# Kernel tuning notes

Hardware: AMD Instinct MI355X
Metric: run time of the kernel (lower is better)

Reference implementation:

```python
import jax, jax.numpy as jnp
import numpy as np

B, T, DM, DFE, DH, DRH = 32, 2048, 128, 64, 64, 64
E, NF, NSF, TOPK = 8, 16, 64, 2
LN_EPS = 1e-5


def setup_inputs() -> dict:
    key = jax.random.key(0)
    ks = jax.random.split(key, 18)
    s = 0.05
    # base expert i owns columns [16*i, 16*i+16); scale=2 -> expert e uses base e//2
    expert_idx = jnp.asarray(np.stack([np.arange(NF) + NF * (e // 2) for e in range(E)]), dtype=jnp.int32)  # [E,NF]
    stage_idx = jnp.arange(NSF, dtype=jnp.int32)  # stage uses all 64 columns
    return {
        'hidden': jax.random.normal(ks[0], (B, T, DM), jnp.float32),
        'feat': jax.random.normal(ks[1], (B, T, NSF), jnp.float32),
        'ln_g': jnp.ones((DM,), jnp.float32),
        'ln_b': jnp.zeros((DM,), jnp.float32),
        'Wp': jax.random.normal(ks[2], (NSF, DFE), jnp.float32) * s,
        'bp': jnp.zeros((DFE,), jnp.float32),
        'Wr1': jax.random.normal(ks[3], (DM + DFE, DRH), jnp.float32) * s,
        'br1': jnp.zeros((DRH,), jnp.float32),
        'Wr2': jax.random.normal(ks[4], (DRH, E), jnp.float32) * s,
        'br2': jnp.zeros((E,), jnp.float32),
        'Wf': jax.random.normal(ks[5], (E, NF, DFE), jnp.float32) * s,
        'bf': jnp.zeros((E, DFE), jnp.float32),
        'We1h': jax.random.normal(ks[6], (E, DM, DH), jnp.float32) * s,
        'We1f': jax.random.normal(ks[7], (E, DFE, DH), jnp.float32) * s,
        'be1': jnp.zeros((E, DH), jnp.float32),
        'We2': jax.random.normal(ks[8], (E, DH, DM), jnp.float32) * s,
        'be2': jnp.zeros((E, DM), jnp.float32),
        'alpha': jnp.asarray(1.0, jnp.float32),
        'item_seq_len': jax.random.randint(ks[9], (B,), 1, T + 1),
        'expert_idx': expert_idx,
        'stage_idx': stage_idx,
    }


def _layernorm(x, g, b):
    mu = jnp.mean(x, -1, keepdims=True)
    v = jnp.mean(jnp.square(x - mu), -1, keepdims=True)
    return (x - mu) * jax.lax.rsqrt(v + LN_EPS) * g + b


def reference(hidden, feat, ln_g, ln_b, Wp, bp, Wr1, br1, Wr2, br2,
              Wf, bf, We1h, We1f, be1, We2, be2, alpha,
              item_seq_len, expert_idx, stage_idx):
    h = _layernorm(hidden, ln_g, ln_b)                         # [B,T,DM]  pre_ln
    femb = feat[..., stage_idx] @ Wp + bp                      # [B,T,DFE] stage feature projection
    # --- token router: MLP -> softmax(temp=1) -> top-k renormalized gates ---
    rin = jnp.concatenate([h, femb], -1)                       # [B,T,DM+DFE]
    logits = jax.nn.relu(rin @ Wr1 + br1) @ Wr2 + br2          # [B,T,E]
    probs = jax.nn.softmax(logits, axis=-1)
    topv, topi = jax.lax.top_k(probs, TOPK)                    # [B,T,K]
    topv = topv / jnp.sum(topv, -1, keepdims=True)
    gates = jnp.sum(jax.nn.one_hot(topi, E, dtype=probs.dtype) * topv[..., None], axis=-2)  # [B,T,E]
    valid = jnp.arange(T)[None, :] < item_seq_len[:, None]     # [B,T]
    gates = gates * valid[..., None].astype(gates.dtype)
    # --- experts: per-expert feature gather + 2-layer GELU MLP (hidden + feat inputs) ---
    ef = feat[:, :, expert_idx]                                # [B,T,E,NF] gather
    x = jnp.einsum('btef,efd->bted', ef, Wf) + bf              # [B,T,E,DFE]
    h1 = jax.nn.gelu(jnp.einsum('btd,edo->bteo', h, We1h)
                     + jnp.einsum('bted,edo->bteo', x, We1f) + be1, approximate=False)
    eo = jnp.einsum('bteo,eod->bted', h1, We2) + be2           # [B,T,E,DM]
    moe = jnp.einsum('bte,bted->btd', gates, eo)               # weighted combine
    next_hidden = hidden + alpha * moe                         # residual, alpha_scale=1, dropout=0
    return next_hidden, gates, probs
```

## Files before the change

kernel.cpp:

```cpp
#include <hip/hip_runtime.h>
#include <hip/hip_bf16.h>


typedef unsigned short u16;
typedef __attribute__((ext_vector_type(8))) short bfrag;
typedef __attribute__((ext_vector_type(8))) u16 u16x8;
typedef __attribute__((ext_vector_type(4))) float facc;
typedef __attribute__((ext_vector_type(4))) float f32x4;

#define NTOK 65536
#define CAP 65536

#define OFF_CNT   ((size_t)0)
#define OFF_LTOK  ((size_t)256)
#define OFF_LGATE (OFF_LTOK + 2097152)
#define OFF_HWS   (OFF_LGATE + 2097152)
#define OFF_W1T   (OFF_HWS + 16777216)
#define OFF_W2T   (OFF_W1T + 196608)
#define OFF_B1P   (OFF_W2T + 131072)
#define OFF_WPR   (OFF_B1P + 2048)
#define OFF_BR1P  (OFF_WPR + 16384)

__device__ __forceinline__ u16 f2bf(float f) {
  union { __hip_bfloat16 h; u16 u; } cv;
  cv.h = __float2bfloat16(f);
  return cv.u;
}

__global__ __launch_bounds__(256)
void k0_pre(const float* __restrict__ Wp, const float* __restrict__ bp,
            const float* __restrict__ Wr1, const float* __restrict__ br1,
            const float* __restrict__ Wf, const float* __restrict__ bfv,
            const float* __restrict__ We1h, const float* __restrict__ We1f,
            const float* __restrict__ be1, const float* __restrict__ We2,
            float* __restrict__ Wpr, float* __restrict__ br1p,
            u16* __restrict__ w1t, u16* __restrict__ w2t, float* __restrict__ b1p)
{
  int j = blockIdx.x * 256 + threadIdx.x;
  if (j < 4096) {
    int i = j >> 6, o = j & 63;
    float s = 0.f;
    for (int k = 0; k < 64; ++k) s += Wp[i*64+k] * Wr1[(128+k)*64 + o];
    Wpr[i*64+o] = s;
  } else if (j < 4160) {
    int o = j - 4096;
    float s = br1[o];
    for (int k = 0; k < 64; ++k) s += bp[k] * Wr1[(128+k)*64 + o];
    br1p[o] = s;
  } else if (j < 4160 + 98304) {
    int idx = j - 4160;
    int e = idx / 12288; int rem = idx % 12288;
    int jj = rem / 192; int k = rem % 192;
    float v = 0.f;
    if (k < 128) v = We1h[(e*128 + k)*64 + jj];
    else if (k < 144) {
      int i = k - 128; float s = 0.f;
      for (int d = 0; d < 64; ++d) s += Wf[(e*16+i)*64 + d] * We1f[(e*64+d)*64 + jj];
      v = s;
    }
    size_t byte = (size_t)(e*64 + jj)*384 + ((2*k) ^ ((jj & 7) << 4));
    *(u16*)((char*)w1t + byte) = f2bf(v);
  } else if (j < 4160 + 98304 + 65536) {
    int idx = j - 4160 - 98304;
    int e = idx / 8192; int rem = idx % 8192;
    int d = rem / 64; int k = rem & 63;
    float v = We2[(e*64 + k)*128 + d];
    size_t byte = (size_t)(e*128 + d)*128 + ((2*k) ^ ((d & 7) << 4));
    *(u16*)((char*)w2t + byte) = f2bf(v);
  } else if (j < 4160 + 98304 + 65536 + 512) {
    int idx = j - 4160 - 98304 - 65536;
    int e = idx >> 6, o = idx & 63;
    float s = be1[e*64 + o];
    for (int d = 0; d < 64; ++d) s += bfv[e*64 + d] * We1f[(e*64+d)*64 + o];
    b1p[e*64 + o] = s;
  }
}

__global__ __launch_bounds__(512)
void k1_router(const float* __restrict__ hidden, const float* __restrict__ feat,
               const float* __restrict__ ln_g, const float* __restrict__ ln_b,
               const float* __restrict__ Wr1, const float* __restrict__ Wr2,
               const float* __restrict__ br2, const int* __restrict__ seqlen,
               const int* __restrict__ sidx_g,
               const float* __restrict__ Wpr, const float* __restrict__ br1p,
               float* __restrict__ outN, float* __restrict__ outG, float* __restrict__ outP,
               u16* __restrict__ hws, int* __restrict__ cnt,
               int* __restrict__ listTok, float* __restrict__ listGate)
{
  __shared__ float At[64*128];
  __shared__ float Wc[64*64];
  __shared__ float sW2[64*8];
  __shared__ float sb1[64], sg[128], sb[128], sbr2[8];
  __shared__ int ssidx[64];
  __shared__ int lcnt[8], lbase[8];
  __shared__ int ltok[8][128];
  __shared__ float lgate[8][128];

  int tid = threadIdx.x;
  int w = tid >> 6, lane = tid & 63;

  if (tid < 512) sW2[tid] = Wr2[tid];
  if (tid < 64) { sb1[tid] = br1p[tid]; ssidx[tid] = sidx_g[tid]; }
  if (tid >= 64 && tid < 192) { int i = tid - 64; sg[i] = ln_g[i]; }
  if (tid >= 192 && tid < 320) { int i = tid - 192; sb[i] = ln_b[i]; }
  if (tid >= 320 && tid < 328) { sbr2[tid-320] = br2[tid-320]; }
  if (tid >= 328 && tid < 336) { lcnt[tid-328] = 0; }
  __syncthreads();

  int tbase = blockIdx.x * 128 + w * 16;

  float h0v[16], h1v[16], fv[16];
  #pragma unroll
  for (int p = 0; p < 8; ++p) {
    int tA = tbase + 2*p, tB = tA + 1;
    float xA0 = hidden[tA*128 + lane],      xA1 = hidden[tA*128 + 64 + lane];
    float xB0 = hidden[tB*128 + lane],      xB1 = hidden[tB*128 + 64 + lane];
    fv[2*p]   = feat[tA*64 + ssidx[lane]];
    fv[2*p+1] = feat[tB*64 + ssidx[lane]];
    outN[tA*128 + lane] = xA0; outN[tA*128 + 64 + lane] = xA1;
    outN[tB*128 + lane] = xB0; outN[tB*128 + 64 + lane] = xB1;
    float sA = xA0 + xA1, sB = xB0 + xB1;
    #pragma unroll
    for (int m = 1; m < 64; m <<= 1) { sA += __shfl_xor(sA, m, 64); sB += __shfl_xor(sB, m, 64); }
    float muA = sA * (1.f/128.f), muB = sB * (1.f/128.f);
    float dA0 = xA0-muA, dA1 = xA1-muA, dB0 = xB0-muB, dB1 = xB1-muB;
    float qA = dA0*dA0 + dA1*dA1, qB = dB0*dB0 + dB1*dB1;
    #pragma unroll
    for (int m = 1; m < 64; m <<= 1) { qA += __shfl_xor(qA, m, 64); qB += __shfl_xor(qB, m, 64); }
    float rsA = rsqrtf(qA*(1.f/128.f) + 1e-5f), rsB = rsqrtf(qB*(1.f/128.f) + 1e-5f);
    float hA0 = dA0*rsA*sg[lane]    + sb[lane],    hA1 = dA1*rsA*sg[64+lane] + sb[64+lane];
    float hB0 = dB0*rsB*sg[lane]    + sb[lane],    hB1 = dB1*rsB*sg[64+lane] + sb[64+lane];
    hws[tA*128 + lane] = f2bf(hA0); hws[tA*128 + 64 + lane] = f2bf(hA1);
    hws[tB*128 + lane] = f2bf(hB0); hws[tB*128 + 64 + lane] = f2bf(hB1);
    h0v[2*p] = hA0; h1v[2*p] = hA1; h0v[2*p+1] = hB0; h1v[2*p+1] = hB1;
  }

  float acc[4][4];
  #pragma unroll
  for (int i = 0; i < 4; ++i)
    #pragma unroll
    for (int q = 0; q < 4; ++q) acc[i][q] = 0.f;

  int tb = w*4 + (lane >> 4);
  int ob = (lane & 15) * 4;

  #pragma unroll 1
  for (int c = 0; c < 3; ++c) {
    __syncthreads();
    const float* wsrc = (c == 0) ? Wr1 : (c == 1) ? (Wr1 + 64*64) : Wpr;
    for (int i = tid; i < 1024; i += 512) ((f32x4*)Wc)[i] = ((const f32x4*)wsrc)[i];
    #pragma unroll
    for (int tk = 0; tk < 16; ++tk) {
      int tl = w*16 + tk;
      float v = (c == 0) ? h0v[tk] : (c == 1) ? h1v[tk] : fv[tk];
      int byte = (lane << 9) + (((((tl >> 2) ^ (lane & 15))) << 4) | ((tl & 3) << 2));
      *(float*)((char*)At + byte) = v;
    }
    __syncthreads();
    #pragma unroll 4
    for (int k = 0; k < 64; ++k) {
      f32x4 a4 = *(const f32x4*)((const char*)At + (k << 9) + ((tb ^ (k & 15)) << 4));
      f32x4 b4 = *(const f32x4*)(Wc + k*64 + ob);
      #pragma unroll
      for (int i = 0; i < 4; ++i)
        #pragma unroll
        for (int q = 0; q < 4; ++q)
          acc[i][q] = fmaf(a4[i], b4[q], acc[i][q]);
    }
  }

  float w2r[4][8];
  #pragma unroll
  for (int q = 0; q < 4; ++q)
    #pragma unroll
    for (int e = 0; e < 8; ++e) w2r[q][e] = sW2[(ob + q)*8 + e];
  float b1r[4];
  #pragma unroll
  for (int q = 0; q < 4; ++q) b1r[q] = sb1[ob + q];

  int j = lane & 15;
  #pragma unroll 1
  for (int ti = 0; ti < 4; ++ti) {
    float lo[8];
    #pragma unroll
    for (int e = 0; e < 8; ++e) lo[e] = 0.f;
    #pragma unroll
    for (int q = 0; q < 4; ++q) {
      float z = fmaxf(acc[ti][q] + b1r[q], 0.f);
      #pragma unroll
      for (int e = 0; e < 8; ++e) lo[e] = fmaf(z, w2r[q][e], lo[e]);
    }
    #pragma unroll
    for (int m = 1; m < 16; m <<= 1) {
      #pragma unroll
      for (int e = 0; e < 8; ++e) lo[e] += __shfl_xor(lo[e], m, 64);
    }
    #pragma unroll
    for (int e = 0; e < 8; ++e) lo[e] += sbr2[e];

    int t = tbase + (lane >> 4)*4 + ti;
    float mx = lo[0];
    #pragma unroll
    for (int e = 1; e < 8; ++e) mx = fmaxf(mx, lo[e]);
    float ex[8]; float s = 0.f;
    #pragma unroll
    for (int e = 0; e < 8; ++e) { ex[e] = __expf(lo[e] - mx); s += ex[e]; }
    float inv = 1.f / s;
    float p[8];
    #pragma unroll
    for (int e = 0; e < 8; ++e) p[e] = ex[e] * inv;
    float p1 = p[0]; int i1 = 0;
    #pragma unroll
    for (int e = 1; e < 8; ++e) { bool tk2 = p[e] > p1; p1 = tk2 ? p[e] : p1; i1 = tk2 ? e : i1; }
    float p2 = -1.f; int i2 = 0;
    #pragma unroll
    for (int e = 0; e < 8; ++e) { bool tk2 = (e != i1) && (p[e] > p2); p2 = tk2 ? p[e] : p2; i2 = tk2 ? e : i2; }
    int bb = t >> 11, tt = t & 2047;
    bool valid = tt < seqlen[bb];
    float gden = 1.f / (p1 + p2);
    float g1 = p1 * gden, g2 = p2 * gden;
    float pv = p[0];
    #pragma unroll
    for (int e = 1; e < 8; ++e) pv = (j == e) ? p[e] : pv;
    if (j < 8) outP[t*8 + j] = pv;
    float gv = (j == i1) ? g1 : ((j == i2) ? g2 : 0.f);
    if (!valid) gv = 0.f;
    if (j < 8) outG[t*8 + j] = gv;
    if (valid && j == 0) {
      int lp = atomicAdd(&lcnt[i1], 1); ltok[i1][lp] = t; lgate[i1][lp] = g1;
      lp = atomicAdd(&lcnt[i2], 1); ltok[i2][lp] = t; lgate[i2][lp] = g2;
    }
  }

  __syncthreads();
  if (tid < 8) lbase[tid] = atomicAdd(&cnt[tid], lcnt[tid]);
  __syncthreads();
  #pragma unroll 1
  for (int e = 0; e < 8; ++e) {
    int ncnt = lcnt[e];
    if (tid < ncnt) {
      listTok[e*CAP + lbase[e] + tid] = ltok[e][tid];
      listGate[e*CAP + lbase[e] + tid] = lgate[e][tid];
    }
  }
}

__global__ __launch_bounds__(256)
void k2_experts(const float* __restrict__ feat, const u16* __restrict__ hws,
                const u16* __restrict__ w1t, const u16* __restrict__ w2t,
                const float* __restrict__ b1p, const float* __restrict__ be2,
                const float* __restrict__ alphap, const int* __restrict__ eidx_g,
                const int* __restrict__ cnt, const int* __restrict__ listTok,
                const float* __restrict__ listGate, float* __restrict__ outN)
{
  __shared__ u16 Xs[64*192];
  __shared__ u16 W1s[64*192];
  __shared__ u16 W2s[128*64];
  __shared__ u16 H1s[64*64];
  __shared__ float b1s[64], be2s[128], gts[64];
  __shared__ int toks[64];
  __shared__ int seidx[16];

  int e = blockIdx.x >> 10;
  int seg = blockIdx.x & 1023;
  int n = cnt[e];
  int row0 = seg << 6;
  if (row0 >= n) return;
  int nr = n - row0; if (nr > 64) nr = 64;
  int tid = threadIdx.x;

  if (tid < 64) {
    int tok = 0; float gt = 0.f;
    if (tid < nr) { tok = listTok[e*CAP + row0 + tid]; gt = listGate[e*CAP + row0 + tid]; }
    toks[tid] = tok; gts[tid] = gt;
    b1s[tid] = b1p[e*64 + tid];
  }
  if (tid >= 64 && tid < 192) be2s[tid - 64] = be2[e*128 + tid - 64];
  if (tid < 16) seidx[tid] = eidx_g[e*16 + tid];
  {
    const u16x8* s1 = (const u16x8*)(w1t + e*64*192);
    u16x8* d1 = (u16x8*)W1s;
    for (int i = tid; i < 1536; i += 256) d1[i] = s1[i];
    const u16x8* s2 = (const u16x8*)(w2t + e*128*64);
    u16x8* d2 = (u16x8*)W2s;
    for (int i = tid; i < 1024; i += 256) d2[i] = s2[i];
  }
  __syncthreads();
  for (int c = tid; c < 1024; c += 256) {
    int r = c >> 4, p = c & 15;
    u16x8 v = *(const u16x8*)(hws + toks[r]*128 + p*8);
    *(u16x8*)((char*)Xs + r*384 + ((p*16) ^ ((r & 7) << 4))) = v;
  }
  if (tid < 128) {
    int r = tid >> 1, hf = tid & 1;
    int tok = toks[r];
    u16x8 ov;
    #pragma unroll
    for (int q = 0; q < 8; ++q) ov[q] = f2bf(feat[tok*64 + seidx[hf*8 + q]]);
    *(u16x8*)((char*)Xs + r*384 + ((256 + hf*16) ^ ((r & 7) << 4))) = ov;
    u16x8 zv = {0,0,0,0,0,0,0,0};
    *(u16x8*)((char*)Xs + r*384 + ((288 + hf*16) ^ ((r & 7) << 4))) = zv;
  }
  __syncthreads();

  int w = tid >> 6, lane = tid & 63;
  int la = lane & 15, lg = lane >> 4;
  int wm = (w >> 1) * 32, wn = (w & 1) * 32;

  facc acc[2][2];
  #pragma unroll
  for (int a = 0; a < 2; ++a)
    #pragma unroll
    for (int b2 = 0; b2 < 2; ++b2) { facc z = {0.f,0.f,0.f,0.f}; acc[a][b2] = z; }
  #pragma unroll
  for (int kc = 0; kc < 5; ++kc) {
    int kb = kc*64 + lg*16;
    bfrag af[2], bf2[2];
    #pragma unroll
    for (int mi = 0; mi < 2; ++mi) {
      int r = wm + mi*16 + la;
      af[mi] = *(const bfrag*)((const char*)Xs + r*384 + (kb ^ ((r & 7) << 4)));
    }
    #pragma unroll
    for (int ni = 0; ni < 2; ++ni) {
      int r = wn + ni*16 + la;
      bf2[ni] = *(const bfrag*)((const char*)W1s + r*384 + (kb ^ ((r & 7) << 4)));
    }
    #pragma unroll
    for (int mi = 0; mi < 2; ++mi)
      #pragma unroll
      for (int ni = 0; ni < 2; ++ni)
        acc[mi][ni] = __builtin_amdgcn_mfma_f32_16x16x32_bf16(af[mi], bf2[ni], acc[mi][ni], 0, 0, 0);
  }
  #pragma unroll
  for (int mi = 0; mi < 2; ++mi)
    #pragma unroll
    for (int ni = 0; ni < 2; ++ni)
      #pragma unroll
      for (int rg = 0; rg < 4; ++rg) {
        int r = wm + mi*16 + lg*4 + rg;
        int c = wn + ni*16 + la;
        float z = acc[mi][ni][rg] + b1s[c];
        float gl = 0.5f * z * (1.f + erff(z * 0.70710678118f));
        *(u16*)((char*)H1s + r*128 + ((2*c) ^ ((r & 7) << 4))) = f2bf(gl);
      }
  __syncthreads();

  facc acc2[2][4];
  #pragma unroll
  for (int a = 0; a < 2; ++a)
    #pragma unroll
    for (int b2 = 0; b2 < 4; ++b2) { facc z = {0.f,0.f,0.f,0.f}; acc2[a][b2] = z; }
  int wn2 = (w & 1) * 64;
  #pragma unroll
  for (int kc = 0; kc < 2; ++kc) {
    int kb = kc*64 + lg*16;
    bfrag af[2], bf2[4];
    #pragma unroll
    for (int mi = 0; mi < 2; ++mi) {
      int r = wm + mi*16 + la;
      af[mi] = *(const bfrag*)((const char*)H1s + r*128 + (kb ^ ((r & 7) << 4)));
    }
    #pragma unroll
    for (int ni = 0; ni < 4; ++ni) {
      int r = wn2 + ni*16 + la;
      bf2[ni] = *(const bfrag*)((const char*)W2s + r*128 + (kb ^ ((r & 7) << 4)));
    }
    #pragma unroll
    for (int mi = 0; mi < 2; ++mi)
      #pragma unroll
      for (int ni = 0; ni < 4; ++ni)
        acc2[mi][ni] = __builtin_amdgcn_mfma_f32_16x16x32_bf16(af[mi], bf2[ni], acc2[mi][ni], 0, 0, 0);
  }
  float alpha = alphap[0];
  #pragma unroll
  for (int mi = 0; mi < 2; ++mi)
    #pragma unroll
    for (int ni = 0; ni < 4; ++ni)
      #pragma unroll
      for (int rg = 0; rg < 4; ++rg) {
        int r = wm + mi*16 + lg*4 + rg;
        int c = wn2 + ni*16 + la;
        float gt = gts[r];
        if (gt != 0.f) {
          float v = acc2[mi][ni][rg] + be2s[c];
          atomicAdd(outN + toks[r]*128 + c, alpha * gt * v);
        }
      }
}

extern "C" void kernel_launch(void* const* d_in, const int* in_sizes, int n_in,
                              void* d_out, int out_size, void* d_ws, size_t ws_size,
                              hipStream_t stream) {
  const float* hidden = (const float*)d_in[0];
  const float* feat   = (const float*)d_in[1];
  const float* ln_g   = (const float*)d_in[2];
  const float* ln_b   = (const float*)d_in[3];
  const float* Wp     = (const float*)d_in[4];
  const float* bp     = (const float*)d_in[5];
  const float* Wr1    = (const float*)d_in[6];
  const float* br1    = (const float*)d_in[7];
  const float* Wr2    = (const float*)d_in[8];
  const float* br2    = (const float*)d_in[9];
  const float* Wf     = (const float*)d_in[10];
  const float* bfv    = (const float*)d_in[11];
  const float* We1h   = (const float*)d_in[12];
  const float* We1f   = (const float*)d_in[13];
  const float* be1    = (const float*)d_in[14];
  const float* We2    = (const float*)d_in[15];
  const float* be2    = (const float*)d_in[16];
  const float* alpha  = (const float*)d_in[17];
  const int* seqlen   = (const int*)d_in[18];
  const int* eidx     = (const int*)d_in[19];
  const int* sidx     = (const int*)d_in[20];

  char* ws = (char*)d_ws;
  int*   cnt      = (int*)(ws + OFF_CNT);
  int*   listTok  = (int*)(ws + OFF_LTOK);
  float* listGate = (float*)(ws + OFF_LGATE);
  u16*   hws      = (u16*)(ws + OFF_HWS);
  u16*   w1t      = (u16*)(ws + OFF_W1T);
  u16*   w2t      = (u16*)(ws + OFF_W2T);
  float* b1p      = (float*)(ws + OFF_B1P);
  float* Wpr      = (float*)(ws + OFF_WPR);
  float* br1p     = (float*)(ws + OFF_BR1P);

  float* outN = (float*)d_out;
  float* outG = outN + (size_t)NTOK * 128;
  float* outP = outG + (size_t)NTOK * 8;

  hipMemsetAsync(ws + OFF_CNT, 0, 256, stream);
  k0_pre<<<659, 256, 0, stream>>>(Wp, bp, Wr1, br1, Wf, bfv, We1h, We1f, be1, We2,
                                  Wpr, br1p, w1t, w2t, b1p);
  k1_router<<<512, 512, 0, stream>>>(hidden, feat, ln_g, ln_b, Wr1, Wr2, br2, seqlen,
                                     sidx, Wpr, br1p, outN, outG, outP, hws, cnt,
                                     listTok, listGate);
  k2_experts<<<8192, 256, 0, stream>>>(feat, hws, w1t, w2t, b1p, be2, alpha, eidx,
                                       cnt, listTok, listGate, outN);
}
```

Measured before the change: 111.2 us.

## Replace atomic MoE scatter with per-slot expert outputs and separate combine kernel

```diff
diff --git a/kernel.cpp b/kernel.cpp
--- a/kernel.cpp
+++ b/kernel.cpp
@@ -12,10 +12,12 @@
 #define CAP 65536
 
 #define OFF_CNT   ((size_t)0)
-#define OFF_LTOK  ((size_t)256)
-#define OFF_LGATE (OFF_LTOK + 2097152)
-#define OFF_HWS   (OFF_LGATE + 2097152)
-#define OFF_W1T   (OFF_HWS + 16777216)
+#define OFF_SEGM  ((size_t)256)
+#define OFF_LTOK  ((size_t)512)
+#define OFF_SMAPG (OFF_LTOK + (size_t)8*CAP*4)
+#define OFF_HWS   (OFF_SMAPG + (size_t)NTOK*8)
+#define OFF_EOTOK (OFF_HWS + (size_t)NTOK*128*2)
+#define OFF_W1T   (OFF_EOTOK + (size_t)NTOK*2*128*2)
 #define OFF_W2T   (OFF_W1T + 196608)
 #define OFF_B1P   (OFF_W2T + 131072)
 #define OFF_WPR   (OFF_B1P + 2048)
@@ -25,6 +27,9 @@
   union { __hip_bfloat16 h; u16 u; } cv;
   cv.h = __float2bfloat16(f);
   return cv.u;
+}
+__device__ __forceinline__ float bf2f(u16 u) {
+  return __uint_as_float(((unsigned)u) << 16);
 }
 
 __global__ __launch_bounds__(256)
@@ -76,119 +81,139 @@
   }
 }
 
-__global__ __launch_bounds__(512)
+__global__ __launch_bounds__(256, 4)
 void k1_router(const float* __restrict__ hidden, const float* __restrict__ feat,
                const float* __restrict__ ln_g, const float* __restrict__ ln_b,
                const float* __restrict__ Wr1, const float* __restrict__ Wr2,
                const float* __restrict__ br2, const int* __restrict__ seqlen,
                const int* __restrict__ sidx_g,
                const float* __restrict__ Wpr, const float* __restrict__ br1p,
-               float* __restrict__ outN, float* __restrict__ outG, float* __restrict__ outP,
+               float* __restrict__ outG, float* __restrict__ outP,
                u16* __restrict__ hws, int* __restrict__ cnt,
-               int* __restrict__ listTok, float* __restrict__ listGate)
+               int* __restrict__ listTok, float* __restrict__ smapG)
 {
-  __shared__ float At[64*128];
+  __shared__ float At[64*64];
   __shared__ float Wc[64*64];
-  __shared__ float sW2[64*8];
+  __shared__ float sW2[512];
   __shared__ float sb1[64], sg[128], sb[128], sbr2[8];
   __shared__ int ssidx[64];
   __shared__ int lcnt[8], lbase[8];
-  __shared__ int ltok[8][128];
-  __shared__ float lgate[8][128];
+  __shared__ int ltok[8][64];
+  __shared__ float tg[64][2];
 
   int tid = threadIdx.x;
-  int w = tid >> 6, lane = tid & 63;
-
-  if (tid < 512) sW2[tid] = Wr2[tid];
+  for (int i = tid; i < 512; i += 256) sW2[i] = Wr2[i];
+  if (tid < 128) sg[tid] = ln_g[tid]; else sb[tid-128] = ln_b[tid-128];
   if (tid < 64) { sb1[tid] = br1p[tid]; ssidx[tid] = sidx_g[tid]; }
-  if (tid >= 64 && tid < 192) { int i = tid - 64; sg[i] = ln_g[i]; }
-  if (tid >= 192 && tid < 320) { int i = tid - 192; sb[i] = ln_b[i]; }
-  if (tid >= 320 && tid < 328) { sbr2[tid-320] = br2[tid-320]; }
-  if (tid >= 328 && tid < 336) { lcnt[tid-328] = 0; }
+  if (tid >= 64 && tid < 72) sbr2[tid-64] = br2[tid-64];
+  if (tid >= 72 && tid < 80) lcnt[tid-72] = 0;
   __syncthreads();
 
-  int tbase = blockIdx.x * 128 + w * 16;
-
-  float h0v[16], h1v[16], fv[16];
-  #pragma unroll
-  for (int p = 0; p < 8; ++p) {
-    int tA = tbase + 2*p, tB = tA + 1;
-    float xA0 = hidden[tA*128 + lane],      xA1 = hidden[tA*128 + 64 + lane];
-    float xB0 = hidden[tB*128 + lane],      xB1 = hidden[tB*128 + 64 + lane];
-    fv[2*p]   = feat[tA*64 + ssidx[lane]];
-    fv[2*p+1] = feat[tB*64 + ssidx[lane]];
-    outN[tA*128 + lane] = xA0; outN[tA*128 + 64 + lane] = xA1;
-    outN[tB*128 + lane] = xB0; outN[tB*128 + 64 + lane] = xB1;
-    float sA = xA0 + xA1, sB = xB0 + xB1;
-    #pragma unroll
-    for (int m = 1; m < 64; m <<= 1) { sA += __shfl_xor(sA, m, 64); sB += __shfl_xor(sB, m, 64); }
-    float muA = sA * (1.f/128.f), muB = sB * (1.f/128.f);
-    float dA0 = xA0-muA, dA1 = xA1-muA, dB0 = xB0-muB, dB1 = xB1-muB;
-    float qA = dA0*dA0 + dA1*dA1, qB = dB0*dB0 + dB1*dB1;
-    #pragma unroll
-    for (int m = 1; m < 64; m <<= 1) { qA += __shfl_xor(qA, m, 64); qB += __shfl_xor(qB, m, 64); }
-    float rsA = rsqrtf(qA*(1.f/128.f) + 1e-5f), rsB = rsqrtf(qB*(1.f/128.f) + 1e-5f);
-    float hA0 = dA0*rsA*sg[lane]    + sb[lane],    hA1 = dA1*rsA*sg[64+lane] + sb[64+lane];
-    float hB0 = dB0*rsB*sg[lane]    + sb[lane],    hB1 = dB1*rsB*sg[64+lane] + sb[64+lane];
-    hws[tA*128 + lane] = f2bf(hA0); hws[tA*128 + 64 + lane] = f2bf(hA1);
-    hws[tB*128 + lane] = f2bf(hB0); hws[tB*128 + 64 + lane] = f2bf(hB1);
-    h0v[2*p] = hA0; h1v[2*p] = hA1; h0v[2*p+1] = hB0; h1v[2*p+1] = hB1;
-  }
+  int tok = tid >> 2, q = tid & 3;
+  int t = blockIdx.x * 64 + tok;
+
+  f32x4 x[8];
+  #pragma unroll
+  for (int i = 0; i < 8; ++i) x[i] = *(const f32x4*)(hidden + (size_t)t*128 + q*32 + i*4);
+  float s = 0.f;
+  #pragma unroll
+  for (int i = 0; i < 8; ++i) { s += x[i][0] + x[i][1]; s += x[i][2] + x[i][3]; }
+  s += __shfl_xor(s, 1, 64); s += __shfl_xor(s, 2, 64);
+  float mu = s * (1.f/128.f);
+  float v = 0.f;
+  #pragma unroll
+  for (int i = 0; i < 8; ++i) {
+    #pragma unroll
+    for (int j = 0; j < 4; ++j) { float d = x[i][j] - mu; v = fmaf(d, d, v); }
+  }
+  v += __shfl_xor(v, 1, 64); v += __shfl_xor(v, 2, 64);
+  float rs = rsqrtf(v * (1.f/128.f) + 1e-5f);
+  #pragma unroll
+  for (int i = 0; i < 8; ++i) {
+    #pragma unroll
+    for (int j = 0; j < 4; ++j) {
+      int c = q*32 + i*4 + j;
+      x[i][j] = (x[i][j] - mu) * rs * sg[c] + sb[c];
+    }
+  }
+  #pragma unroll
+  for (int m = 0; m < 4; ++m) {
+    u16x8 o;
+    #pragma unroll
+    for (int j = 0; j < 4; ++j) { o[j] = f2bf(x[2*m][j]); o[4+j] = f2bf(x[2*m+1][j]); }
+    *(u16x8*)(hws + (size_t)t*128 + q*32 + m*8) = o;
+  }
+  float fv[16];
+  #pragma unroll
+  for (int i = 0; i < 16; ++i) fv[i] = feat[(size_t)t*64 + ssidx[q*16 + i]];
 
   float acc[4][4];
   #pragma unroll
   for (int i = 0; i < 4; ++i)
     #pragma unroll
-    for (int q = 0; q < 4; ++q) acc[i][q] = 0.f;
-
-  int tb = w*4 + (lane >> 4);
-  int ob = (lane & 15) * 4;
+    for (int p = 0; p < 4; ++p) acc[i][p] = 0.f;
+
+  int tb = tid >> 4;
+  int ob = (tid & 15) * 4;
 
   #pragma unroll 1
   for (int c = 0; c < 3; ++c) {
     __syncthreads();
-    const float* wsrc = (c == 0) ? Wr1 : (c == 1) ? (Wr1 + 64*64) : Wpr;
-    for (int i = tid; i < 1024; i += 512) ((f32x4*)Wc)[i] = ((const f32x4*)wsrc)[i];
-    #pragma unroll
-    for (int tk = 0; tk < 16; ++tk) {
-      int tl = w*16 + tk;
-      float v = (c == 0) ? h0v[tk] : (c == 1) ? h1v[tk] : fv[tk];
-      int byte = (lane << 9) + (((((tl >> 2) ^ (lane & 15))) << 4) | ((tl & 3) << 2));
-      *(float*)((char*)At + byte) = v;
-    }
+    if (c < 2) {
+      if ((c == 0) ? (q < 2) : (q >= 2)) {
+        int kbase = (c == 0) ? q*32 : (q-2)*32;
+        #pragma unroll
+        for (int i = 0; i < 8; ++i)
+          #pragma unroll
+          for (int j = 0; j < 4; ++j) {
+            int kr = kbase + i*4 + j;
+            int byte = (kr << 8) + ((((tok >> 2) ^ ((kr >> 2) & 15)) << 4) | ((tok & 3) << 2));
+            *(float*)((char*)At + byte) = x[i][j];
+          }
+      }
+    } else {
+      #pragma unroll
+      for (int i = 0; i < 16; ++i) {
+        int kr = q*16 + i;
+        int byte = (kr << 8) + ((((tok >> 2) ^ ((kr >> 2) & 15)) << 4) | ((tok & 3) << 2));
+        *(float*)((char*)At + byte) = fv[i];
+      }
+    }
+    const float* wsrc = (c == 0) ? Wr1 : (c == 1) ? (Wr1 + 4096) : Wpr;
+    for (int i = tid; i < 1024; i += 256) ((f32x4*)Wc)[i] = ((const f32x4*)wsrc)[i];
     __syncthreads();
     #pragma unroll 4
     for (int k = 0; k < 64; ++k) {
-      f32x4 a4 = *(const f32x4*)((const char*)At + (k << 9) + ((tb ^ (k & 15)) << 4));
+      f32x4 a4 = *(const f32x4*)((const char*)At + (k << 8) + ((tb ^ ((k >> 2) & 15)) << 4));
       f32x4 b4 = *(const f32x4*)(Wc + k*64 + ob);
       #pragma unroll
       for (int i = 0; i < 4; ++i)
         #pragma unroll
-        for (int q = 0; q < 4; ++q)
-          acc[i][q] = fmaf(a4[i], b4[q], acc[i][q]);
+        for (int p = 0; p < 4; ++p)
+          acc[i][p] = fmaf(a4[i], b4[p], acc[i][p]);
     }
   }
 
   float w2r[4][8];
   #pragma unroll
-  for (int q = 0; q < 4; ++q)
-    #pragma unroll
-    for (int e = 0; e < 8; ++e) w2r[q][e] = sW2[(ob + q)*8 + e];
+  for (int p = 0; p < 4; ++p)
+    #pragma unroll
+    for (int e = 0; e < 8; ++e) w2r[p][e] = sW2[(ob + p)*8 + e];
   float b1r[4];
   #pragma unroll
-  for (int q = 0; q < 4; ++q) b1r[q] = sb1[ob + q];
-
-  int j = lane & 15;
+  for (int p = 0; p < 4; ++p) b1r[p] = sb1[ob + p];
+
+  int j16 = tid & 15;
   #pragma unroll 1
   for (int ti = 0; ti < 4; ++ti) {
     float lo[8];
     #pragma unroll
     for (int e = 0; e < 8; ++e) lo[e] = 0.f;
     #pragma unroll
-    for (int q = 0; q < 4; ++q) {
-      float z = fmaxf(acc[ti][q] + b1r[q], 0.f);
-      #pragma unroll
-      for (int e = 0; e < 8; ++e) lo[e] = fmaf(z, w2r[q][e], lo[e]);
+    for (int p = 0; p < 4; ++p) {
+      float z = fmaxf(acc[ti][p] + b1r[p], 0.f);
+      #pragma unroll
+      for (int e = 0; e < 8; ++e) lo[e] = fmaf(z, w2r[p][e], lo[e]);
     }
     #pragma unroll
     for (int m = 1; m < 16; m <<= 1) {
@@ -198,14 +223,15 @@
     #pragma unroll
     for (int e = 0; e < 8; ++e) lo[e] += sbr2[e];
 
-    int t = tbase + (lane >> 4)*4 + ti;
+    int tloc = tb*4 + ti;
+    int tt = blockIdx.x*64 + tloc;
     float mx = lo[0];
     #pragma unroll
     for (int e = 1; e < 8; ++e) mx = fmaxf(mx, lo[e]);
-    float ex[8]; float s = 0.f;
-    #pragma unroll
-    for (int e = 0; e < 8; ++e) { ex[e] = __expf(lo[e] - mx); s += ex[e]; }
-    float inv = 1.f / s;
+    float ex[8]; float ss = 0.f;
+    #pragma unroll
+    for (int e = 0; e < 8; ++e) { ex[e] = __expf(lo[e] - mx); ss += ex[e]; }
+    float inv = 1.f / ss;
     float p[8];
     #pragma unroll
     for (int e = 0; e < 8; ++e) p[e] = ex[e] * inv;
@@ -215,20 +241,24 @@
     float p2 = -1.f; int i2 = 0;
     #pragma unroll
     for (int e = 0; e < 8; ++e) { bool tk2 = (e != i1) && (p[e] > p2); p2 = tk2 ? p[e] : p2; i2 = tk2 ? e : i2; }
-    int bb = t >> 11, tt = t & 2047;
-    bool valid = tt < seqlen[bb];
+    bool valid = (tt & 2047) < seqlen[tt >> 11];
     float gden = 1.f / (p1 + p2);
     float g1 = p1 * gden, g2 = p2 * gden;
     float pv = p[0];
     #pragma unroll
-    for (int e = 1; e < 8; ++e) pv = (j == e) ? p[e] : pv;
-    if (j < 8) outP[t*8 + j] = pv;
-    float gv = (j == i1) ? g1 : ((j == i2) ? g2 : 0.f);
+    for (int e = 1; e < 8; ++e) pv = (j16 == e) ? p[e] : pv;
+    if (j16 < 8) outP[(size_t)tt*8 + j16] = pv;
+    float gv = (j16 == i1) ? g1 : ((j16 == i2) ? g2 : 0.f);
     if (!valid) gv = 0.f;
-    if (j < 8) outG[t*8 + j] = gv;
-    if (valid && j == 0) {
-      int lp = atomicAdd(&lcnt[i1], 1); ltok[i1][lp] = t; lgate[i1][lp] = g1;
-      lp = atomicAdd(&lcnt[i2], 1); ltok[i2][lp] = t; lgate[i2][lp] = g2;
+    if (j16 < 8) outG[(size_t)tt*8 + j16] = gv;
+    if (j16 == 0) {
+      if (valid) {
+        int lp = atomicAdd(&lcnt[i1], 1); ltok[i1][lp] = (tt << 1);
+        lp = atomicAdd(&lcnt[i2], 1);     ltok[i2][lp] = (tt << 1) | 1;
+        tg[tloc][0] = g1; tg[tloc][1] = g2;
+      } else {
+        tg[tloc][0] = 0.f; tg[tloc][1] = 0.f;
+      }
     }
   }
 
@@ -238,10 +268,21 @@
   #pragma unroll 1
   for (int e = 0; e < 8; ++e) {
     int ncnt = lcnt[e];
-    if (tid < ncnt) {
-      listTok[e*CAP + lbase[e] + tid] = ltok[e][tid];
-      listGate[e*CAP + lbase[e] + tid] = lgate[e][tid];
-    }
+    if (tid < ncnt) listTok[(size_t)e*CAP + lbase[e] + tid] = ltok[e][tid];
+  }
+  if (tid < 64) {
+    float2 g; g.x = tg[tid][0]; g.y = tg[tid][1];
+    ((float2*)smapG)[blockIdx.x*64 + tid] = g;
+  }
+}
+
+__global__ void k1b_prefix(const int* __restrict__ cnt, int* __restrict__ segm)
+{
+  if (threadIdx.x == 0 && blockIdx.x == 0) {
+    int s = 0;
+    #pragma unroll
+    for (int e = 0; e < 8; ++e) { segm[e] = s; s += (cnt[e] + 63) >> 6; }
+    segm[8] = s;
   }
 }
 
@@ -249,34 +290,38 @@
 void k2_experts(const float* __restrict__ feat, const u16* __restrict__ hws,
                 const u16* __restrict__ w1t, const u16* __restrict__ w2t,
                 const float* __restrict__ b1p, const float* __restrict__ be2,
-                const float* __restrict__ alphap, const int* __restrict__ eidx_g,
-                const int* __restrict__ cnt, const int* __restrict__ listTok,
-                const float* __restrict__ listGate, float* __restrict__ outN)
+                const int* __restrict__ eidx_g, const int* __restrict__ cnt,
+                const int* __restrict__ segm, const int* __restrict__ listTok,
+                u16* __restrict__ eoTok)
 {
   __shared__ u16 Xs[64*192];
   __shared__ u16 W1s[64*192];
   __shared__ u16 W2s[128*64];
   __shared__ u16 H1s[64*64];
-  __shared__ float b1s[64], be2s[128], gts[64];
-  __shared__ int toks[64];
+  __shared__ float b1s[64], be2s[128];
+  __shared__ int sent[64];
   __shared__ int seidx[16];
-
-  int e = blockIdx.x >> 10;
-  int seg = blockIdx.x & 1023;
+  __shared__ int snr;
+
+  int b = blockIdx.x;
+  if (b >= segm[8]) return;
+  int e = 0;
+  #pragma unroll
+  for (int i = 1; i < 8; ++i) if (b >= segm[i]) e = i;
+  int row0 = (b - segm[e]) << 6;
   int n = cnt[e];
-  int row0 = seg << 6;
-  if (row0 >= n) return;
   int nr = n - row0; if (nr > 64) nr = 64;
   int tid = threadIdx.x;
+  if (tid == 0) snr = nr;
 
   if (tid < 64) {
-    int tok = 0; float gt = 0.f;
-    if (tid < nr) { tok = listTok[e*CAP + row0 + tid]; gt = listGate[e*CAP + row0 + tid]; }
-    toks[tid] = tok; gts[tid] = gt;
+    int ent = 0;
+    if (tid < nr) ent = listTok[(size_t)e*CAP + row0 + tid];
+    sent[tid] = ent;
     b1s[tid] = b1p[e*64 + tid];
   }
   if (tid >= 64 && tid < 192) be2s[tid - 64] = be2[e*128 + tid - 64];
-  if (tid < 16) seidx[tid] = eidx_g[e*16 + tid];
+  if (tid >= 192 && tid < 208) seidx[tid-192] = eidx_g[e*16 + tid - 192];
   {
     const u16x8* s1 = (const u16x8*)(w1t + e*64*192);
     u16x8* d1 = (u16x8*)W1s;
@@ -288,15 +333,15 @@
   __syncthreads();
   for (int c = tid; c < 1024; c += 256) {
     int r = c >> 4, p = c & 15;
-    u16x8 v = *(const u16x8*)(hws + toks[r]*128 + p*8);
+    u16x8 v = *(const u16x8*)(hws + (size_t)(sent[r] >> 1)*128 + p*8);
     *(u16x8*)((char*)Xs + r*384 + ((p*16) ^ ((r & 7) << 4))) = v;
   }
   if (tid < 128) {
     int r = tid >> 1, hf = tid & 1;
-    int tok = toks[r];
+    int tk = sent[r] >> 1;
     u16x8 ov;
     #pragma unroll
-    for (int q = 0; q < 8; ++q) ov[q] = f2bf(feat[tok*64 + seidx[hf*8 + q]]);
+    for (int p = 0; p < 8; ++p) ov[p] = f2bf(feat[(size_t)tk*64 + seidx[hf*8 + p]]);
     *(u16x8*)((char*)Xs + r*384 + ((256 + hf*16) ^ ((r & 7) << 4))) = ov;
     u16x8 zv = {0,0,0,0,0,0,0,0};
     *(u16x8*)((char*)Xs + r*384 + ((288 + hf*16) ^ ((r & 7) << 4))) = zv;
@@ -372,7 +417,6 @@
       for (int ni = 0; ni < 4; ++ni)
         acc2[mi][ni] = __builtin_amdgcn_mfma_f32_16x16x32_bf16(af[mi], bf2[ni], acc2[mi][ni], 0, 0, 0);
   }
-  float alpha = alphap[0];
   #pragma unroll
   for (int mi = 0; mi < 2; ++mi)
     #pragma unroll
@@ -381,12 +425,43 @@
       for (int rg = 0; rg < 4; ++rg) {
         int r = wm + mi*16 + lg*4 + rg;
         int c = wn2 + ni*16 + la;
-        float gt = gts[r];
-        if (gt != 0.f) {
+        if (r < snr) {
           float v = acc2[mi][ni][rg] + be2s[c];
-          atomicAdd(outN + toks[r]*128 + c, alpha * gt * v);
+          eoTok[(size_t)sent[r]*128 + c] = f2bf(v);
         }
       }
+}
+
+__global__ __launch_bounds__(256)
+void k3_combine(const float* __restrict__ hidden, const float* __restrict__ smapG,
+                const u16* __restrict__ eoTok, const float* __restrict__ alphap,
+                float* __restrict__ outN)
+{
+  int tid = threadIdx.x;
+  int tok = tid >> 2, q = tid & 3;
+  int t = blockIdx.x*64 + tok;
+  float2 g = ((const float2*)smapG)[t];
+  float a = alphap[0];
+  float ag0 = a * g.x, ag1 = a * g.y;
+  const f32x4* hp = (const f32x4*)(hidden + (size_t)t*128 + q*32);
+  f32x4* op = (f32x4*)(outN + (size_t)t*128 + q*32);
+  const u16x8* e0 = (const u16x8*)(eoTok + ((size_t)t*2)*128 + q*32);
+  const u16x8* e1 = (const u16x8*)(eoTok + ((size_t)t*2 + 1)*128 + q*32);
+  #pragma unroll
+  for (int i = 0; i < 4; ++i) {
+    f32x4 r0 = hp[2*i], r1 = hp[2*i+1];
+    if (g.x != 0.f) {
+      u16x8 x0 = e0[i];
+      #pragma unroll
+      for (int j = 0; j < 4; ++j) { r0[j] = fmaf(ag0, bf2f(x0[j]), r0[j]); r1[j] = fmaf(ag0, bf2f(x0[4+j]), r1[j]); }
+    }
+    if (g.y != 0.f) {
+      u16x8 x1 = e1[i];
+      #pragma unroll
+      for (int j = 0; j < 4; ++j) { r0[j] = fmaf(ag1, bf2f(x1[j]), r0[j]); r1[j] = fmaf(ag1, bf2f(x1[4+j]), r1[j]); }
+    }
+    op[2*i] = r0; op[2*i+1] = r1;
+  }
 }
 
 extern "C" void kernel_launch(void* const* d_in, const int* in_sizes, int n_in,
@@ -416,9 +491,11 @@
 
   char* ws = (char*)d_ws;
   int*   cnt      = (int*)(ws + OFF_CNT);
+  int*   segm     = (int*)(ws + OFF_SEGM);
   int*   listTok  = (int*)(ws + OFF_LTOK);
-  float* listGate = (float*)(ws + OFF_LGATE);
+  float* smapG    = (float*)(ws + OFF_SMAPG);
   u16*   hws      = (u16*)(ws + OFF_HWS);
+  u16*   eoTok    = (u16*)(ws + OFF_EOTOK);
   u16*   w1t      = (u16*)(ws + OFF_W1T);
   u16*   w2t      = (u16*)(ws + OFF_W2T);
   float* b1p      = (float*)(ws + OFF_B1P);
@@ -432,9 +509,11 @@
   hipMemsetAsync(ws + OFF_CNT, 0, 256, stream);
   k0_pre<<<659, 256, 0, stream>>>(Wp, bp, Wr1, br1, Wf, bfv, We1h, We1f, be1, We2,
                                   Wpr, br1p, w1t, w2t, b1p);
-  k1_router<<<512, 512, 0, stream>>>(hidden, feat, ln_g, ln_b, Wr1, Wr2, br2, seqlen,
-                                     sidx, Wpr, br1p, outN, outG, outP, hws, cnt,
-                                     listTok, listGate);
-  k2_experts<<<8192, 256, 0, stream>>>(feat, hws, w1t, w2t, b1p, be2, alpha, eidx,
-                                       cnt, listTok, listGate, outN);
-}
+  k1_router<<<1024, 256, 0, stream>>>(hidden, feat, ln_g, ln_b, Wr1, Wr2, br2, seqlen,
+                                      sidx, Wpr, br1p, outG, outP, hws, cnt,
+                                      listTok, smapG);
+  k1b_prefix<<<1, 64, 0, stream>>>(cnt, segm);
+  k2_experts<<<2056, 256, 0, stream>>>(feat, hws, w1t, w2t, b1p, be2, eidx,
+                                       cnt, segm, listTok, eoTok);
+  k3_combine<<<1024, 256, 0, stream>>>(hidden, smapG, eoTok, alpha, outN);
+}
```

Result: slower. 129.8 us (+16.7%).
